# Optimization experiments

Hardware: AMD Instinct MI355X
Metric: run time of the kernel (lower is better)

## Reference

```python
import jax, jax.numpy as jnp
import numpy as np

B, H, L, D, S = 32, 1, 4096, 64, 512  # batch, heads(=1, codebook shared), seq, d_k, n_code
PE_LAM = 100000.0
EPS = 1e-6


def _sinusoid_embs(length, width, lam):
    # standard sinusoid table [length, width]: concat(sin, cos)
    pos = jnp.arange(length, dtype=jnp.float32)
    inv_lams = lam ** (-jnp.arange(0, width, 2, dtype=jnp.float32) / width)
    pre = pos[:, None] * inv_lams[None, :]
    return jnp.concatenate([jnp.sin(pre), jnp.cos(pre)], axis=-1)


def _codebook():
    # get_codebook: sinusoids -> rms-norm (center/gain/bias off) -> tau^{-1/2} scale -> stop-grad -> [1,S,D]
    c = _sinusoid_embs(S, D, PE_LAM)
    c = c * jax.lax.rsqrt(jnp.mean(jnp.square(c), axis=-1, keepdims=True) + EPS)
    tau = float(D) ** 0.5
    return jax.lax.stop_gradient((tau ** -0.5) * c)[None, ...]  # [H=1, S, D]


def setup_inputs() -> dict:
    key = jax.random.key(0)
    vecs = jax.random.normal(key, (B, H, L, D), dtype=jnp.float32)
    loss_mask = jnp.ones((B, L), dtype=jnp.float32)
    return {"vecs": vecs, "loss_mask": loss_mask}


def reference(vecs, loss_mask):
    c = _codebook()  # [1, S, D]
    # pairwise squared distances [B,H,L,S] via ||v||^2 - 2 v.c + ||c||^2
    diffs2 = (
        jnp.sum(jnp.square(vecs), axis=-1)[..., None]
        - 2.0 * jnp.einsum("bhlk,hsk->bhls", vecs, c)
        + jnp.sum(jnp.square(c), axis=-1)[None, :, None, :]
    )
    z = jnp.argmin(diffs2, axis=-1).astype(jnp.int32)       # [B,H,L]
    errs2 = jax.nn.relu(jnp.min(diffs2, axis=-1))           # [B,H,L]
    # gather codewords: codebook [1,1,S,D], indices [B,H,L,1]
    cz = jnp.take_along_axis(c[None, ...], z[..., None], axis=2)  # [B,H,L,D]
    # straight-through estimator
    quantized = jax.lax.stop_gradient(cz) + vecs - jax.lax.stop_gradient(vecs)
    # l_commit = mean over (B,L) of sum over heads of masked errs2
    l_commit = jnp.mean(jnp.sum(loss_mask[:, None, :] * errs2, axis=1))
    return quantized, z, l_commit, errs2
```

## Files before the change

### kernel.cpp

```cpp
#include <hip/hip_runtime.h>
#include <math.h>

#define NB 32
#define NL 4096
#define ND 64
#define NS 512
#define NTOK (NB*NL)

#define OFF_Q 0
#define OFF_Z (NTOK*ND)
#define OFF_LC (OFF_Z + NTOK)
#define OFF_E (OFF_LC + 1)

typedef __attribute__((ext_vector_type(8))) short short8;
typedef __attribute__((ext_vector_type(4))) float f32x4;
typedef unsigned int u32;
typedef unsigned short u16;
typedef unsigned long long u64;

#define QCODES 128
#define TOKS 128
#define TPB 512
#define SLOTS 12
#define SLOTP 13
#define EPS_H 1e-3f
#define NBLK (NTOK / TOKS)

__device__ __forceinline__ u32 f2bf_rne(float x) {
    u32 u = __float_as_uint(x);
    return (u + 0x7fffu + ((u >> 16) & 1u)) >> 16;
}

__device__ __forceinline__ void upd_key(u64& best, float dist, int code) {
    u32 u = __float_as_uint(dist);
    u ^= (u >> 31) ? 0xFFFFFFFFu : 0x80000000u;
    u64 k = ((u64)u << 32) | (u32)code;
    if (k < best) best = k;
}

__global__ void cb_kernel(float* __restrict__ cb, float* __restrict__ cc,
                          u16* __restrict__ cbh, u16* __restrict__ cbl) {
    int s = blockIdx.x;
    int d = threadIdx.x;
    int j = (d < 32) ? d : (d - 32);
    double e = -(double)(2 * j) / 64.0;
    double invlam = pow(100000.0, e);
    double pre = (double)s * invlam;
    float val = (float)((d < 32) ? sin(pre) : cos(pre));

    float sq = val * val;
    #pragma unroll
    for (int off = 32; off > 0; off >>= 1) sq += __shfl_xor(sq, off);
    float mean = sq * (1.0f / 64.0f);
    float scale = (1.0f / sqrtf(mean + 1e-6f)) * 0.35355339059327379f;
    float c = val * scale;
    cb[s * ND + d] = c;

    float c2 = c * c;
    #pragma unroll
    for (int off = 32; off > 0; off >>= 1) c2 += __shfl_xor(c2, off);
    if (d == 0) cc[s] = c2;

    u32 hb = f2bf_rne(c);
    float hf = __uint_as_float(hb << 16);
    u32 lb = f2bf_rne(c - hf);
    int g = d >> 3, ee = d & 7;
    int pos = s * 64 + (((g ^ (s & 7)) << 3) | ee);
    cbh[pos] = (u16)hb;
    cbl[pos] = (u16)lb;
}

__launch_bounds__(TPB, 4)
__global__ void fused_kernel(const float* __restrict__ vecs,
                             const float* __restrict__ mask,
                             const float* __restrict__ cb,
                             const float* __restrict__ cc,
                             const u16* __restrict__ cbh,
                             const u16* __restrict__ cbl,
                             float* __restrict__ outq,
                             float* __restrict__ outz,
                             float* __restrict__ oute,
                             float* __restrict__ partial) {
    __shared__ float4 svec[TOKS * 16];
    __shared__ u16 ldsH[QCODES * 64];
    __shared__ u16 ldsL[QCODES * 64];
    __shared__ u32 slots[TOKS * SLOTP];
    __shared__ float hval[TOKS * SLOTP];
    __shared__ u32 cnt_l[TOKS];
    __shared__ int z_l[TOKS];
    __shared__ float wsum[TPB / 64];

    const int tid = threadIdx.x;
    const int grp = blockIdx.x;
    const int w = tid >> 6;
    const int lane = tid & 63;
    const int c16 = lane & 15;
    const int h = lane >> 4;

    {
        const float4* vsrc = (const float4*)(vecs + (size_t)grp * TOKS * ND);
        #pragma unroll
        for (int i = 0; i < 4; ++i) {
            int idx = i * TPB + tid;
            int row = idx >> 4, g = idx & 15;
            svec[row * 16 + (g ^ (row & 15))] = vsrc[idx];
        }
        if (tid < TOKS) cnt_l[tid] = 0;
    }
    #pragma unroll
    for (int i = 0; i < 2; ++i) {
        int k = i * TPB + tid;
        ((short8*)ldsH)[k] = ((const short8*)cbh)[k];
        ((short8*)ldsL)[k] = ((const short8*)cbl)[k];
    }
    __syncthreads();

    const int trow = w * 16 + c16;
    short8 bh[2], bl[2];
    #pragma unroll
    for (int kk = 0; kk < 2; ++kk) {
        float x[8];
        #pragma unroll
        for (int u = 0; u < 2; ++u) {
            int g = kk * 8 + h * 2 + u;
            float4 t = svec[trow * 16 + (g ^ (trow & 15))];
            x[u * 4 + 0] = t.x; x[u * 4 + 1] = t.y;
            x[u * 4 + 2] = t.z; x[u * 4 + 3] = t.w;
        }
        short8 H, L;
        #pragma unroll
        for (int e2 = 0; e2 < 8; ++e2) {
            u32 hb = f2bf_rne(x[e2]);
            float hf = __uint_as_float(hb << 16);
            u32 lb = f2bf_rne(x[e2] - hf);
            H[e2] = (short)hb; L[e2] = (short)lb;
        }
        bh[kk] = H; bl[kk] = L;
    }

    for (int q = 0; q < 4; ++q) {
        if (q) {
            __syncthreads();
            #pragma unroll
            for (int i = 0; i < 2; ++i) {
                int k = i * TPB + tid;
                ((short8*)ldsH)[k] = ((const short8*)(cbh + q * QCODES * 64))[k];
                ((short8*)ldsL)[k] = ((const short8*)(cbl + q * QCODES * 64))[k];
            }
            __syncthreads();
        }
        #pragma unroll
        for (int c = 0; c < 2; ++c) {
            f32x4 acc[4];
            #pragma unroll
            for (int mt = 0; mt < 4; ++mt) {
                int cr = q * QCODES + c * 64 + mt * 16 + h * 4;
                f32x4 ini;
                ini[0] = -0.5f * cc[cr + 0];
                ini[1] = -0.5f * cc[cr + 1];
                ini[2] = -0.5f * cc[cr + 2];
                ini[3] = -0.5f * cc[cr + 3];
                acc[mt] = ini;
            }
            #pragma unroll
            for (int mt = 0; mt < 4; ++mt) {
                int code_l = c * 64 + mt * 16 + c16;
                int sw = code_l & 7;
                short8 ah[2], al[2];
                #pragma unroll
                for (int kk = 0; kk < 2; ++kk) {
                    int off = code_l * 64 + (((kk * 4 + h) ^ sw) << 3);
                    ah[kk] = *(const short8*)(ldsH + off);
                    al[kk] = *(const short8*)(ldsL + off);
                }
                #pragma unroll
                for (int kk = 0; kk < 2; ++kk) {
                    acc[mt] = __builtin_amdgcn_mfma_f32_16x16x32_bf16(ah[kk], bh[kk], acc[mt], 0, 0, 0);
                    acc[mt] = __builtin_amdgcn_mfma_f32_16x16x32_bf16(ah[kk], bl[kk], acc[mt], 0, 0, 0);
                    acc[mt] = __builtin_amdgcn_mfma_f32_16x16x32_bf16(al[kk], bh[kk], acc[mt], 0, 0, 0);
                }
            }
            float m = acc[0][0];
            #pragma unroll
            for (int mt = 0; mt < 4; ++mt) {
                m = fmaxf(m, fmaxf(fmaxf(acc[mt][0], acc[mt][1]),
                                   fmaxf(acc[mt][2], acc[mt][3])));
            }
            m = fmaxf(m, __shfl_xor(m, 16));
            m = fmaxf(m, __shfl_xor(m, 32));
            float thr = m - EPS_H;
            #pragma unroll
            for (int mt = 0; mt < 4; ++mt) {
                #pragma unroll
                for (int r = 0; r < 4; ++r) {
                    float v = acc[mt][r];
                    if (v >= thr) {
                        u32 pos = atomicAdd(&cnt_l[trow], 1u);
                        if (pos < (u32)SLOTS) {
                            slots[trow * SLOTP + pos] = (u32)(q * QCODES + c * 64 + mt * 16 + h * 4 + r);
                            hval[trow * SLOTP + pos] = v;
                        }
                    }
                }
            }
        }
    }
    __syncthreads();

    const int p  = tid >> 2;
    const int qs = tid & 3;
    const int tok = grp * TOKS + p;

    float4 vf[16];
    #pragma unroll
    for (int g = 0; g < 16; ++g) vf[g] = svec[p * 16 + (g ^ (p & 15))];
    float vv;
    {
        float a0 = 0.f, a1 = 0.f, a2 = 0.f, a3 = 0.f;
        #pragma unroll
        for (int i = 0; i < 16; ++i) {
            a0 = fmaf(vf[i].x, vf[i].x, a0);
            a1 = fmaf(vf[i].y, vf[i].y, a1);
            a2 = fmaf(vf[i].z, vf[i].z, a2);
            a3 = fmaf(vf[i].w, vf[i].w, a3);
        }
        vv = (a0 + a1) + (a2 + a3);
    }

    u32 cnt = cnt_l[p]; if (cnt > (u32)SLOTS) cnt = (u32)SLOTS;
    float hm = -3.4e38f;
    for (u32 j2 = 0; j2 < cnt; ++j2) hm = fmaxf(hm, hval[p * SLOTP + j2]);
    float thr2 = hm - EPS_H;

    u64 best = 0xFFFFFFFFFFFFFFFFull;
    for (u32 j2 = qs; j2 < cnt; j2 += 4) {
        if (hval[p * SLOTP + j2] >= thr2) {
            int code = (int)slots[p * SLOTP + j2];
            const float4* cs = (const float4*)(cb + (size_t)code * ND);
            float d0 = 0.f, d1 = 0.f, d2 = 0.f, d3 = 0.f;
            #pragma unroll
            for (int i2 = 0; i2 < 16; ++i2) {
                float4 cv = cs[i2];
                d0 = fmaf(cv.x, vf[i2].x, d0);
                d1 = fmaf(cv.y, vf[i2].y, d1);
                d2 = fmaf(cv.z, vf[i2].z, d2);
                d3 = fmaf(cv.w, vf[i2].w, d3);
            }
            float dot = (d0 + d1) + (d2 + d3);
            float dist = (vv - 2.0f * dot) + cc[code];
            upd_key(best, dist, code);
        }
    }
    {
        u64 o = __shfl_xor(best, 1); if (o < best) best = o;
        o = __shfl_xor(best, 2); if (o < best) best = o;
    }

    float contrib = 0.0f;
    if (qs == 0) {
        int zi = (int)(best & 0xFFFFFFFFu);
        u32 du = (u32)(best >> 32);
        du ^= (du >> 31) ? 0x80000000u : 0xFFFFFFFFu;
        float dmin = __uint_as_float(du);
        float err = fmaxf(dmin, 0.0f);
        outz[tok] = (float)zi;
        oute[tok] = err;
        z_l[p] = zi;
        contrib = mask[tok] * err;
    }
    #pragma unroll
    for (int off = 32; off > 0; off >>= 1) contrib += __shfl_xor(contrib, off);
    if (lane == 0) wsum[w] = contrib;
    __syncthreads();
    if (tid == 0) {
        float t = 0.f;
        #pragma unroll
        for (int i = 0; i < TPB / 64; ++i) t += wsum[i];
        partial[grp] = t;
    }

    const float4* cb4 = (const float4*)cb;
    float4* qo = (float4*)(outq + (size_t)grp * TOKS * ND);
    #pragma unroll
    for (int i = 0; i < 4; ++i) {
        int gidx = i * TPB + tid;
        int t2 = gidx >> 4;
        int sub = gidx & 15;
        qo[gidx] = cb4[(size_t)z_l[t2] * 16 + sub];
    }
}

__global__ void fin_kernel(const float* __restrict__ partial, float* __restrict__ outl) {
    int t = threadIdx.x;
    float x = partial[t];
    #pragma unroll
    for (int off = 32; off > 0; off >>= 1) x += __shfl_xor(x, off);
    __shared__ float ws[16];
    if ((t & 63) == 0) ws[t >> 6] = x;
    __syncthreads();
    if (t == 0) {
        float s = 0.f;
        #pragma unroll
        for (int i = 0; i < 16; ++i) s += ws[i];
        outl[0] = s / (float)NTOK;
    }
}

extern "C" void kernel_launch(void* const* d_in, const int* in_sizes, int n_in,
                              void* d_out, int out_size, void* d_ws, size_t ws_size,
                              hipStream_t stream) {
    const float* vecs = (const float*)d_in[0];
    const float* mask = (const float*)d_in[1];

    float* out = (float*)d_out;
    float* outq = out + OFF_Q;
    float* outz = out + OFF_Z;
    float* outl = out + OFF_LC;
    float* oute = out + OFF_E;

    float* ws_f = (float*)d_ws;
    float* cb = ws_f;
    float* cc = ws_f + 32768;
    u16*  cbh = (u16*)(ws_f + 33280);
    u16*  cbl = (u16*)(ws_f + 49664);
    float* partial = ws_f + 66048;

    cb_kernel<<<NS, 64, 0, stream>>>(cb, cc, cbh, cbl);
    fused_kernel<<<NBLK, TPB, 0, stream>>>(vecs, mask, cb, cc, cbh, cbl,
                                           outq, outz, oute, partial);
    fin_kernel<<<1, 1024, 0, stream>>>(partial, outl);
}
```

Baseline: 68.52 us.

## Register-block 4 token tiles per wave to reuse codebook LDS fragments across MFMAs

Each wave now owns 64 tokens (four 16-token MFMA tiles) instead of 16. Every codebook fragment read from LDS feeds four tiles, which cuts LDS traffic and per-token codebook staging. Blocks grow to 256 tokens with 256 threads. Vectors are loaded straight from global memory instead of through a shared tile, and the code norms are cached in LDS. The exact rescoring moves to one thread per token, with a full 512-code fallback when more than the slot limit of candidates collide. The cost is much higher register pressure, fewer blocks in the grid, and a serial refine loop per thread.

```diff
diff --git a/kernel.cpp b/kernel.cpp
--- a/kernel.cpp
+++ b/kernel.cpp
@@ -19,10 +19,10 @@
 typedef unsigned long long u64;
 
 #define QCODES 128
-#define TOKS 128
-#define TPB 512
-#define SLOTS 12
-#define SLOTP 13
+#define TOKS 256
+#define TPB 256
+#define SLOTS 16
+#define SLOTP 17
 #define EPS_H 1e-3f
 #define NBLK (NTOK / TOKS)
 
@@ -36,6 +36,23 @@
     u ^= (u >> 31) ? 0xFFFFFFFFu : 0x80000000u;
     u64 k = ((u64)u << 32) | (u32)code;
     if (k < best) best = k;
+}
+
+__device__ __forceinline__ float dist_code(const float* __restrict__ cb,
+                                           const float* __restrict__ ccs,
+                                           const float4* vf, float vv, int code) {
+    const float4* cs = (const float4*)(cb + (size_t)code * ND);
+    float d0 = 0.f, d1 = 0.f, d2 = 0.f, d3 = 0.f;
+    #pragma unroll
+    for (int i = 0; i < 16; ++i) {
+        float4 cv = cs[i];
+        d0 = fmaf(cv.x, vf[i].x, d0);
+        d1 = fmaf(cv.y, vf[i].y, d1);
+        d2 = fmaf(cv.z, vf[i].z, d2);
+        d3 = fmaf(cv.w, vf[i].w, d3);
+    }
+    float dot = (d0 + d1) + (d2 + d3);
+    return (vv - 2.0f * dot) + ccs[code];
 }
 
 __global__ void cb_kernel(float* __restrict__ cb, float* __restrict__ cc,
@@ -70,7 +87,7 @@
     cbl[pos] = (u16)lb;
 }
 
-__launch_bounds__(TPB, 4)
+__launch_bounds__(TPB, 2)
 __global__ void fused_kernel(const float* __restrict__ vecs,
                              const float* __restrict__ mask,
                              const float* __restrict__ cb,
@@ -81,11 +98,11 @@
                              float* __restrict__ outz,
                              float* __restrict__ oute,
                              float* __restrict__ partial) {
-    __shared__ float4 svec[TOKS * 16];
     __shared__ u16 ldsH[QCODES * 64];
     __shared__ u16 ldsL[QCODES * 64];
     __shared__ u32 slots[TOKS * SLOTP];
     __shared__ float hval[TOKS * SLOTP];
+    __shared__ float ccs[NS];
     __shared__ u32 cnt_l[TOKS];
     __shared__ int z_l[TOKS];
     __shared__ float wsum[TPB / 64];
@@ -97,52 +114,44 @@
     const int c16 = lane & 15;
     const int h = lane >> 4;
 
-    {
-        const float4* vsrc = (const float4*)(vecs + (size_t)grp * TOKS * ND);
-        #pragma unroll
-        for (int i = 0; i < 4; ++i) {
-            int idx = i * TPB + tid;
-            int row = idx >> 4, g = idx & 15;
-            svec[row * 16 + (g ^ (row & 15))] = vsrc[idx];
-        }
-        if (tid < TOKS) cnt_l[tid] = 0;
-    }
-    #pragma unroll
-    for (int i = 0; i < 2; ++i) {
+    #pragma unroll
+    for (int i = 0; i < 4; ++i) {
         int k = i * TPB + tid;
         ((short8*)ldsH)[k] = ((const short8*)cbh)[k];
         ((short8*)ldsL)[k] = ((const short8*)cbl)[k];
     }
+    ccs[tid] = cc[tid];
+    ccs[tid + 256] = cc[tid + 256];
+    cnt_l[tid] = 0;
+
+    short8 bh[4][2], bl[4][2];
+    const int tokbase = grp * TOKS + w * 64;
+    #pragma unroll
+    for (int nt = 0; nt < 4; ++nt) {
+        const float* vp = vecs + (size_t)(tokbase + nt * 16 + c16) * ND;
+        #pragma unroll
+        for (int kk = 0; kk < 2; ++kk) {
+            const float4* p = (const float4*)(vp + kk * 32 + h * 8);
+            float4 t0 = p[0], t1 = p[1];
+            float x[8] = {t0.x, t0.y, t0.z, t0.w, t1.x, t1.y, t1.z, t1.w};
+            short8 H, L;
+            #pragma unroll
+            for (int e2 = 0; e2 < 8; ++e2) {
+                u32 hb = f2bf_rne(x[e2]);
+                float hf = __uint_as_float(hb << 16);
+                u32 lb = f2bf_rne(x[e2] - hf);
+                H[e2] = (short)hb; L[e2] = (short)lb;
+            }
+            bh[nt][kk] = H; bl[nt][kk] = L;
+        }
+    }
     __syncthreads();
-
-    const int trow = w * 16 + c16;
-    short8 bh[2], bl[2];
-    #pragma unroll
-    for (int kk = 0; kk < 2; ++kk) {
-        float x[8];
-        #pragma unroll
-        for (int u = 0; u < 2; ++u) {
-            int g = kk * 8 + h * 2 + u;
-            float4 t = svec[trow * 16 + (g ^ (trow & 15))];
-            x[u * 4 + 0] = t.x; x[u * 4 + 1] = t.y;
-            x[u * 4 + 2] = t.z; x[u * 4 + 3] = t.w;
-        }
-        short8 H, L;
-        #pragma unroll
-        for (int e2 = 0; e2 < 8; ++e2) {
-            u32 hb = f2bf_rne(x[e2]);
-            float hf = __uint_as_float(hb << 16);
-            u32 lb = f2bf_rne(x[e2] - hf);
-            H[e2] = (short)hb; L[e2] = (short)lb;
-        }
-        bh[kk] = H; bl[kk] = L;
-    }
 
     for (int q = 0; q < 4; ++q) {
         if (q) {
             __syncthreads();
             #pragma unroll
-            for (int i = 0; i < 2; ++i) {
+            for (int i = 0; i < 4; ++i) {
                 int k = i * TPB + tid;
                 ((short8*)ldsH)[k] = ((const short8*)(cbh + q * QCODES * 64))[k];
                 ((short8*)ldsL)[k] = ((const short8*)(cbl + q * QCODES * 64))[k];
@@ -151,16 +160,17 @@
         }
         #pragma unroll
         for (int c = 0; c < 2; ++c) {
-            f32x4 acc[4];
+            f32x4 acc[4][4];
             #pragma unroll
             for (int mt = 0; mt < 4; ++mt) {
                 int cr = q * QCODES + c * 64 + mt * 16 + h * 4;
                 f32x4 ini;
-                ini[0] = -0.5f * cc[cr + 0];
-                ini[1] = -0.5f * cc[cr + 1];
-                ini[2] = -0.5f * cc[cr + 2];
-                ini[3] = -0.5f * cc[cr + 3];
-                acc[mt] = ini;
+                ini[0] = -0.5f * ccs[cr + 0];
+                ini[1] = -0.5f * ccs[cr + 1];
+                ini[2] = -0.5f * ccs[cr + 2];
+                ini[3] = -0.5f * ccs[cr + 3];
+                #pragma unroll
+                for (int nt = 0; nt < 4; ++nt) acc[mt][nt] = ini;
             }
             #pragma unroll
             for (int mt = 0; mt < 4; ++mt) {
@@ -174,31 +184,38 @@
                     al[kk] = *(const short8*)(ldsL + off);
                 }
                 #pragma unroll
-                for (int kk = 0; kk < 2; ++kk) {
-                    acc[mt] = __builtin_amdgcn_mfma_f32_16x16x32_bf16(ah[kk], bh[kk], acc[mt], 0, 0, 0);
-                    acc[mt] = __builtin_amdgcn_mfma_f32_16x16x32_bf16(ah[kk], bl[kk], acc[mt], 0, 0, 0);
-                    acc[mt] = __builtin_amdgcn_mfma_f32_16x16x32_bf16(al[kk], bh[kk], acc[mt], 0, 0, 0);
+                for (int nt = 0; nt < 4; ++nt) {
+                    #pragma unroll
+                    for (int kk = 0; kk < 2; ++kk) {
+                        acc[mt][nt] = __builtin_amdgcn_mfma_f32_16x16x32_bf16(ah[kk], bh[nt][kk], acc[mt][nt], 0, 0, 0);
+                        acc[mt][nt] = __builtin_amdgcn_mfma_f32_16x16x32_bf16(ah[kk], bl[nt][kk], acc[mt][nt], 0, 0, 0);
+                        acc[mt][nt] = __builtin_amdgcn_mfma_f32_16x16x32_bf16(al[kk], bh[nt][kk], acc[mt][nt], 0, 0, 0);
+                    }
                 }
             }
-            float m = acc[0][0];
-            #pragma unroll
-            for (int mt = 0; mt < 4; ++mt) {
-                m = fmaxf(m, fmaxf(fmaxf(acc[mt][0], acc[mt][1]),
-                                   fmaxf(acc[mt][2], acc[mt][3])));
-            }
-            m = fmaxf(m, __shfl_xor(m, 16));
-            m = fmaxf(m, __shfl_xor(m, 32));
-            float thr = m - EPS_H;
-            #pragma unroll
-            for (int mt = 0; mt < 4; ++mt) {
-                #pragma unroll
-                for (int r = 0; r < 4; ++r) {
-                    float v = acc[mt][r];
-                    if (v >= thr) {
-                        u32 pos = atomicAdd(&cnt_l[trow], 1u);
-                        if (pos < (u32)SLOTS) {
-                            slots[trow * SLOTP + pos] = (u32)(q * QCODES + c * 64 + mt * 16 + h * 4 + r);
-                            hval[trow * SLOTP + pos] = v;
+            #pragma unroll
+            for (int nt = 0; nt < 4; ++nt) {
+                float m = acc[0][nt][0];
+                #pragma unroll
+                for (int mt = 0; mt < 4; ++mt) {
+                    m = fmaxf(m, fmaxf(fmaxf(acc[mt][nt][0], acc[mt][nt][1]),
+                                       fmaxf(acc[mt][nt][2], acc[mt][nt][3])));
+                }
+                m = fmaxf(m, __shfl_xor(m, 16));
+                m = fmaxf(m, __shfl_xor(m, 32));
+                float thr = m - EPS_H;
+                int tl = w * 64 + nt * 16 + c16;
+                #pragma unroll
+                for (int mt = 0; mt < 4; ++mt) {
+                    #pragma unroll
+                    for (int r = 0; r < 4; ++r) {
+                        float v = acc[mt][nt][r];
+                        if (v >= thr) {
+                            u32 pos = atomicAdd(&cnt_l[tl], 1u);
+                            if (pos < (u32)SLOTS) {
+                                slots[tl * SLOTP + pos] = (u32)(q * QCODES + c * 64 + mt * 16 + h * 4 + r);
+                                hval[tl * SLOTP + pos] = v;
+                            }
                         }
                     }
                 }
@@ -207,13 +224,15 @@
     }
     __syncthreads();
 
-    const int p  = tid >> 2;
-    const int qs = tid & 3;
+    const int p = tid;
     const int tok = grp * TOKS + p;
 
     float4 vf[16];
-    #pragma unroll
-    for (int g = 0; g < 16; ++g) vf[g] = svec[p * 16 + (g ^ (p & 15))];
+    {
+        const float4* vr = (const float4*)(vecs + (size_t)tok * ND);
+        #pragma unroll
+        for (int g = 0; g < 16; ++g) vf[g] = vr[g];
+    }
     float vv;
     {
         float a0 = 0.f, a1 = 0.f, a2 = 0.f, a3 = 0.f;
@@ -227,47 +246,33 @@
         vv = (a0 + a1) + (a2 + a3);
     }
 
-    u32 cnt = cnt_l[p]; if (cnt > (u32)SLOTS) cnt = (u32)SLOTS;
-    float hm = -3.4e38f;
-    for (u32 j2 = 0; j2 < cnt; ++j2) hm = fmaxf(hm, hval[p * SLOTP + j2]);
-    float thr2 = hm - EPS_H;
-
     u64 best = 0xFFFFFFFFFFFFFFFFull;
-    for (u32 j2 = qs; j2 < cnt; j2 += 4) {
-        if (hval[p * SLOTP + j2] >= thr2) {
-            int code = (int)slots[p * SLOTP + j2];
-            const float4* cs = (const float4*)(cb + (size_t)code * ND);
-            float d0 = 0.f, d1 = 0.f, d2 = 0.f, d3 = 0.f;
-            #pragma unroll
-            for (int i2 = 0; i2 < 16; ++i2) {
-                float4 cv = cs[i2];
-                d0 = fmaf(cv.x, vf[i2].x, d0);
-                d1 = fmaf(cv.y, vf[i2].y, d1);
-                d2 = fmaf(cv.z, vf[i2].z, d2);
-                d3 = fmaf(cv.w, vf[i2].w, d3);
-            }
-            float dot = (d0 + d1) + (d2 + d3);
-            float dist = (vv - 2.0f * dot) + cc[code];
-            upd_key(best, dist, code);
-        }
-    }
-    {
-        u64 o = __shfl_xor(best, 1); if (o < best) best = o;
-        o = __shfl_xor(best, 2); if (o < best) best = o;
-    }
-
-    float contrib = 0.0f;
-    if (qs == 0) {
-        int zi = (int)(best & 0xFFFFFFFFu);
-        u32 du = (u32)(best >> 32);
-        du ^= (du >> 31) ? 0x80000000u : 0xFFFFFFFFu;
-        float dmin = __uint_as_float(du);
-        float err = fmaxf(dmin, 0.0f);
-        outz[tok] = (float)zi;
-        oute[tok] = err;
-        z_l[p] = zi;
-        contrib = mask[tok] * err;
-    }
+    u32 cntraw = cnt_l[p];
+    if (cntraw > (u32)SLOTS) {
+        for (int code = 0; code < NS; ++code)
+            upd_key(best, dist_code(cb, ccs, vf, vv, code), code);
+    } else {
+        float hm = -3.4e38f;
+        for (u32 j2 = 0; j2 < cntraw; ++j2) hm = fmaxf(hm, hval[p * SLOTP + j2]);
+        float thr2 = hm - EPS_H;
+        for (u32 j2 = 0; j2 < cntraw; ++j2) {
+            if (hval[p * SLOTP + j2] >= thr2) {
+                int code = (int)slots[p * SLOTP + j2];
+                upd_key(best, dist_code(cb, ccs, vf, vv, code), code);
+            }
+        }
+    }
+
+    int zi = (int)(best & 0xFFFFFFFFu);
+    u32 du = (u32)(best >> 32);
+    du ^= (du >> 31) ? 0x80000000u : 0xFFFFFFFFu;
+    float dmin = __uint_as_float(du);
+    float err = fmaxf(dmin, 0.0f);
+    outz[tok] = (float)zi;
+    oute[tok] = err;
+    z_l[p] = zi;
+    float contrib = mask[tok] * err;
+
     #pragma unroll
     for (int off = 32; off > 0; off >>= 1) contrib += __shfl_xor(contrib, off);
     if (lane == 0) wsum[w] = contrib;
@@ -282,7 +287,7 @@
     const float4* cb4 = (const float4*)cb;
     float4* qo = (float4*)(outq + (size_t)grp * TOKS * ND);
     #pragma unroll
-    for (int i = 0; i < 4; ++i) {
+    for (int i = 0; i < 16; ++i) {
         int gidx = i * TPB + tid;
         int t2 = gidx >> 4;
         int sub = gidx & 15;
@@ -295,13 +300,13 @@
     float x = partial[t];
     #pragma unroll
     for (int off = 32; off > 0; off >>= 1) x += __shfl_xor(x, off);
-    __shared__ float ws[16];
+    __shared__ float ws[8];
     if ((t & 63) == 0) ws[t >> 6] = x;
     __syncthreads();
     if (t == 0) {
         float s = 0.f;
         #pragma unroll
-        for (int i = 0; i < 16; ++i) s += ws[i];
+        for (int i = 0; i < 8; ++i) s += ws[i];
         outl[0] = s / (float)NTOK;
     }
 }
@@ -328,5 +333,5 @@
     cb_kernel<<<NS, 64, 0, stream>>>(cb, cc, cbh, cbl);
     fused_kernel<<<NBLK, TPB, 0, stream>>>(vecs, mask, cb, cc, cbh, cbl,
                                            outq, outz, oute, partial);
-    fin_kernel<<<1, 1024, 0, stream>>>(partial, outl);
-}
+    fin_kernel<<<1, 512, 0, stream>>>(partial, outl);
+}
```

After: 74.06 us. 1.08x slower.
